# Kernel tuning notes

Hardware: AMD Instinct MI355X
Metric: run time of the kernel (lower is better)

The kernel has to match this reference:

```python
import jax, jax.numpy as jnp
import numpy as np

B, S, D, H = 2, 2048, 1024, 16
HD = D // H  # head_dim = 64
NEG = -1.0e9


def setup_inputs() -> dict:
    key = jax.random.key(0)
    ks = jax.random.split(key, 9)
    s = 1.0 / np.sqrt(D)
    return {
        "x": jax.random.normal(ks[0], (B, S, D), jnp.float32),
        "mask": jnp.ones((B, S), jnp.float32),
        "Wq": jax.random.normal(ks[1], (D, D), jnp.float32) * s,
        "bq": jnp.zeros((D,), jnp.float32),
        "Wk": jax.random.normal(ks[2], (D, D), jnp.float32) * s,
        "bk": jnp.zeros((D,), jnp.float32),
        "Wv": jax.random.normal(ks[3], (D, D), jnp.float32) * s,
        "bv": jnp.zeros((D,), jnp.float32),
        "Wo": jax.random.normal(ks[4], (D, D), jnp.float32) * s,
        "bo": jnp.zeros((D,), jnp.float32),
    }


def reference(x, mask, Wq, bq, Wk, bk, Wv, bv, Wo, bo):
    # QKV projections -> [B, H, S, HD]
    def proj(t, W, b):
        return (t @ W + b).reshape(B, S, H, HD).transpose(0, 2, 1, 3)

    q = proj(x, Wq, bq)
    k = proj(x, Wk, bk)
    v = proj(x, Wv, bv)

    scores = jnp.einsum("bhqd,bhkd->bhqk", q, k) / jnp.sqrt(jnp.asarray(HD, x.dtype))
    # causal mask: scores * m + (1-m) * -1e9 (matches original exactly)
    cm = jnp.tril(jnp.ones((S, S), x.dtype))[None, None]
    scores = scores * cm + (1.0 - cm) * NEG
    # 2D padding mask branch
    scores = scores + (1.0 - mask[:, None, None, :]) * NEG

    attn = jax.nn.softmax(scores, axis=-1)
    out = jnp.einsum("bhqk,bhkd->bqhd", attn, v).reshape(B, S, D)
    return out @ Wo + bo
```

## Files before the change

kernel.cpp:

```cpp
#include <hip/hip_runtime.h>
#include <hip/hip_bf16.h>
#include <cstdint>
#include <cstddef>

typedef __attribute__((ext_vector_type(8))) short short8;
typedef __attribute__((ext_vector_type(4))) float floatx4;
typedef __attribute__((ext_vector_type(4))) unsigned short ushortx4;
typedef __attribute__((ext_vector_type(2))) unsigned int uintx2;

#define MFMA16(a, b, c) __builtin_amdgcn_mfma_f32_16x16x32_bf16((a), (b), (c), 0, 0, 0)
#define LOG2E 1.44269504088896340736f
#define EXP2(x) __builtin_amdgcn_exp2f(x)

__device__ __forceinline__ unsigned short f2bf(float f) {
  unsigned int u = __builtin_bit_cast(unsigned int, f);
  u += 0x7fffu + ((u >> 16) & 1u);
  return (unsigned short)(u >> 16);
}

__device__ __forceinline__ unsigned int pk2(float a, float b) {
  float2 f; f.x = a; f.y = b;
  __hip_bfloat162 h = __float22bfloat162_rn(f);
  unsigned int u;
  __builtin_memcpy(&u, &h, 4);
  return u;
}

typedef __attribute__((address_space(1))) void gvoid_t;
typedef __attribute__((address_space(3))) void svoid_t;
__device__ __forceinline__ void gload_lds16(const void* g, void* l) {
  __builtin_amdgcn_global_load_lds((gvoid_t*)(uintptr_t)g, (svoid_t*)(uintptr_t)l, 16, 0, 0);
}

__global__ void convert_x(const float* __restrict__ x, unsigned short* __restrict__ xb) {
  int i = (blockIdx.x * 256 + threadIdx.x) * 4;
  floatx4 v = *(const floatx4*)(x + i);
  uintx2 o;
  o[0] = pk2(v[0], v[1]);
  o[1] = pk2(v[2], v[3]);
  *(uintx2*)(xb + i) = o;
}

__global__ void transpose_w(const float* __restrict__ Wq, const float* __restrict__ Wk,
                            const float* __restrict__ Wv, const float* __restrict__ Wo,
                            unsigned short* __restrict__ Wqkvt, unsigned short* __restrict__ Wot) {
  __shared__ float tile[32][33];
  int z = blockIdx.z;
  const float* W = (z == 0) ? Wq : (z == 1) ? Wk : (z == 2) ? Wv : Wo;
  unsigned short* out = (z == 3) ? Wot : (Wqkvt + (size_t)z * 1024 * 1024);
  int n0 = blockIdx.x * 32, k0 = blockIdx.y * 32;
  int tx = threadIdx.x, ty = threadIdx.y;
#pragma unroll
  for (int j = 0; j < 4; ++j)
    tile[ty + j * 8][tx] = W[(size_t)(k0 + ty + j * 8) * 1024 + n0 + tx];
  __syncthreads();
#pragma unroll
  for (int j = 0; j < 4; ++j)
    out[(size_t)(n0 + ty + j * 8) * 1024 + k0 + tx] = f2bf(tile[tx][ty + j * 8]);
}

#define GEMM_PROLOGUE()                                                        \
  __shared__ __align__(16) unsigned short As[64 * 64];                         \
  __shared__ __align__(16) unsigned short Bs[128 * 64];                        \
  const int tid = threadIdx.x;                                                 \
  const int lane = tid & 63;                                                   \
  const int wid = tid >> 6;                                                    \
  const int col = lane & 15;                                                   \
  const int quad = lane >> 4;                                                  \
  const int m0 = blockIdx.x * 64;                                              \
  const int n0 = blockIdx.y * 128;                                             \
  const int wm = wid >> 1;                                                     \
  const int wn = wid & 1;                                                      \
  floatx4 acc[2][4];                                                           \
  _Pragma("unroll") for (int i = 0; i < 2; ++i)                                \
      _Pragma("unroll") for (int j = 0; j < 4; ++j)                            \
          acc[i][j] = (floatx4)(0.f);                                          \
  _Pragma("unroll 1") for (int kt = 0; kt < 16; ++kt) {                        \
    __syncthreads();                                                           \
    _Pragma("unroll") for (int call = 0; call < 2; ++call) {                   \
      int c = call * 256 + tid;                                                \
      int r = c >> 3, ch = c & 7;                                              \
      gload_lds16(A + (size_t)(m0 + r) * 1024 + kt * 64 + ((ch ^ (r & 7)) * 8),\
                  As + (size_t)(call * 256 + wid * 64) * 8);                   \
    }                                                                          \
    _Pragma("unroll") for (int call = 0; call < 4; ++call) {                   \
      int c = call * 256 + tid;                                                \
      int r = c >> 3, ch = c & 7;                                              \
      gload_lds16(Bt + (size_t)(n0 + r) * 1024 + kt * 64 + ((ch ^ (r & 7)) * 8),\
                  Bs + (size_t)(call * 256 + wid * 64) * 8);                   \
    }                                                                          \
    __syncthreads();                                                           \
    _Pragma("unroll") for (int ks = 0; ks < 2; ++ks) {                         \
      short8 af[2], bf[4];                                                     \
      _Pragma("unroll") for (int rt = 0; rt < 2; ++rt) {                       \
        int row = wm * 32 + rt * 16 + col;                                     \
        af[rt] = *(const short8*)&As[row * 64 + (((ks * 4 + quad) ^ (row & 7)) * 8)]; \
      }                                                                        \
      _Pragma("unroll") for (int ct = 0; ct < 4; ++ct) {                       \
        int row = wn * 64 + ct * 16 + col;                                     \
        bf[ct] = *(const short8*)&Bs[row * 64 + (((ks * 4 + quad) ^ (row & 7)) * 8)]; \
      }                                                                        \
      _Pragma("unroll") for (int rt = 0; rt < 2; ++rt)                         \
          _Pragma("unroll") for (int ct = 0; ct < 4; ++ct)                     \
              acc[rt][ct] = MFMA16(af[rt], bf[ct], acc[rt][ct]);               \
    }                                                                          \
  }

__global__ __launch_bounds__(256, 5)
void gemm_qkv(const unsigned short* __restrict__ A, const unsigned short* __restrict__ Bt,
              const float* __restrict__ bq, const float* __restrict__ bk,
              const float* __restrict__ bv,
              unsigned short* __restrict__ Qo, unsigned short* __restrict__ Ko,
              unsigned short* __restrict__ Vo) {
  GEMM_PROLOGUE()
  const int nseg = n0 >> 10;
  const float* bias = (nseg == 0) ? bq : ((nseg == 1) ? bk : bv);
#pragma unroll
  for (int rt = 0; rt < 2; ++rt) {
#pragma unroll
    for (int ct = 0; ct < 4; ++ct) {
      int mg = m0 + wm * 32 + rt * 16 + quad * 4;
      int ng = n0 + wn * 64 + ct * 16 + col;
      int c = ng & 1023;
      int hh = c >> 6, hd = c & 63;
      int b_ = mg >> 11, s = mg & 2047;
      float bb = bias[c];
      if (nseg == 2) {
        uintx2 pk;
        pk[0] = pk2(acc[rt][ct][0] + bb, acc[rt][ct][1] + bb);
        pk[1] = pk2(acc[rt][ct][2] + bb, acc[rt][ct][3] + bb);
        *(uintx2*)&Vo[(size_t)(b_ * 16 + hh) * 131072 + (size_t)hd * 2048 + s] = pk;
      } else {
        unsigned short* dst =
            ((nseg == 0) ? Qo : Ko) + ((size_t)(b_ * 16 + hh) * 2048 + s) * 64 + hd;
        float scl = (nseg == 0) ? (0.125f * LOG2E) : 1.0f;
#pragma unroll
        for (int i = 0; i < 4; ++i) dst[(size_t)i * 64] = f2bf((acc[rt][ct][i] + bb) * scl);
      }
    }
  }
}

__global__ __launch_bounds__(256, 5)
void gemm_out(const unsigned short* __restrict__ A, const unsigned short* __restrict__ Bt,
              const float* __restrict__ bo, float* __restrict__ Out) {
  GEMM_PROLOGUE()
#pragma unroll
  for (int rt = 0; rt < 2; ++rt) {
#pragma unroll
    for (int ct = 0; ct < 4; ++ct) {
      int mg = m0 + wm * 32 + rt * 16 + quad * 4;
      int ng = n0 + wn * 64 + ct * 16 + col;
      float bb = bo[ng];
#pragma unroll
      for (int i = 0; i < 4; ++i)
        Out[(size_t)(mg + i) * 1024 + ng] = acc[rt][ct][i] + bb;
    }
  }
}

__global__ __launch_bounds__(256, 3)
void flash_attn(const unsigned short* __restrict__ Q, const unsigned short* __restrict__ K,
                const unsigned short* __restrict__ Vt, const float* __restrict__ mask,
                unsigned short* __restrict__ O) {
  __shared__ __align__(16) unsigned short Ks[128 * 64];
  __shared__ __align__(16) unsigned short Vs[64 * 128];
  __shared__ __align__(16) unsigned short Ps[64 * 128];

  const int tid = threadIdx.x;
  const int lane = tid & 63;
  const int wid = tid >> 6;
  const int col = lane & 15;
  const int quad = lane >> 4;
  const int j = 31 - (int)(blockIdx.x >> 5);
  const int bh = blockIdx.x & 31;
  const int b = bh >> 4, h = bh & 15;
  const int q0 = j * 64;
  const int tdiag = j >> 1;

  const unsigned short* Qp = Q + (size_t)bh * 2048 * 64;
  const unsigned short* Kp = K + (size_t)bh * 2048 * 64;
  const unsigned short* Vp = Vt + (size_t)bh * 64 * 2048;
  const float* mp = mask + b * 2048;

  const int lr8 = lane >> 3, lc8 = lane & 7;
  const int lr16 = lane >> 4, lc16 = lane & 15;
  const floatx4 fzero = (floatx4)(0.f);
  const floatx4 fone = (floatx4)(1.f);

#pragma unroll
  for (int i = 0; i < 2; ++i) {
    int seg = wid * 2 + i;
    int r = seg * 8 + lr8;
    gload_lds16(Qp + (size_t)(q0 + r) * 64 + ((lc8 ^ (r & 7)) * 8), Ps + seg * 512);
  }
  __syncthreads();
  short8 qf[2];
  {
    int q = wid * 16 + col;
#pragma unroll
    for (int ks = 0; ks < 2; ++ks)
      qf[ks] = *(const short8*)&Ps[q * 64 + (((ks * 4 + quad) ^ (q & 7)) * 8)];
  }

  floatx4 o[4];
#pragma unroll
  for (int dt = 0; dt < 4; ++dt) o[dt] = fzero;
  float mrow = -1e30f;
  float lrow = 0.f;

#pragma unroll 1
  for (int t = 0; t <= tdiag; ++t) {
    if (t > 0) __syncthreads();
#pragma unroll
    for (int i = 0; i < 4; ++i) {
      int seg = wid * 4 + i;
      int r = seg * 8 + lr8;
      gload_lds16(Kp + (size_t)(t * 128 + r) * 64 + ((lc8 ^ (r & 7)) * 8), Ks + seg * 512);
    }
#pragma unroll
    for (int i = 0; i < 4; ++i) {
      int seg = wid * 4 + i;
      int r = seg * 4 + lr16;
      gload_lds16(Vp + (size_t)r * 2048 + t * 128 + ((lc16 ^ (r & 15)) * 8), Vs + seg * 512);
    }
    __syncthreads();

    floatx4 mbias[8];
#pragma unroll
    for (int rt = 0; rt < 8; ++rt) {
      floatx4 mm = *(const floatx4*)&mp[t * 128 + rt * 16 + quad * 4];
      mbias[rt] = (fone - mm) * (-1.0e9f * LOG2E);
    }

    floatx4 sc[8];
#pragma unroll
    for (int rt = 0; rt < 8; ++rt) {
      int kr = rt * 16 + col;
      short8 kf0 = *(const short8*)&Ks[kr * 64 + ((quad ^ (col & 7)) * 8)];
      short8 kf1 = *(const short8*)&Ks[kr * 64 + (((4 + quad) ^ (col & 7)) * 8)];
      floatx4 s0 = MFMA16(kf0, qf[0], fzero);
      s0 = MFMA16(kf1, qf[1], s0);
      sc[rt] = s0 + mbias[rt];
    }
    if (t == tdiag) {
      int qg = q0 + wid * 16 + col;
#pragma unroll
      for (int rt = 0; rt < 8; ++rt)
#pragma unroll
        for (int i = 0; i < 4; ++i)
          if (t * 128 + rt * 16 + quad * 4 + i > qg) sc[rt][i] = -1.0e9f * LOG2E;
    }

    float mt = -1e30f;
#pragma unroll
    for (int rt = 0; rt < 8; ++rt)
      mt = fmaxf(mt, fmaxf(fmaxf(sc[rt][0], sc[rt][1]), fmaxf(sc[rt][2], sc[rt][3])));
    mt = fmaxf(mt, __shfl_xor(mt, 16));
    mt = fmaxf(mt, __shfl_xor(mt, 32));
    float mn = fmaxf(mrow, mt);
    float alpha = EXP2(mrow - mn);
    mrow = mn;
    float sum = 0.f;
#pragma unroll
    for (int rt = 0; rt < 8; ++rt)
#pragma unroll
      for (int i = 0; i < 4; ++i) {
        float p = EXP2(sc[rt][i] - mn);
        sc[rt][i] = p;
        sum += p;
      }
    sum += __shfl_xor(sum, 16);
    sum += __shfl_xor(sum, 32);
    lrow = lrow * alpha + sum;
#pragma unroll
    for (int dt = 0; dt < 4; ++dt) o[dt] *= alpha;
    {
      int qloc = wid * 16 + col;
#pragma unroll
      for (int rt = 0; rt < 8; ++rt) {
        uintx2 w;
        w[0] = pk2(sc[rt][0], sc[rt][1]);
        w[1] = pk2(sc[rt][2], sc[rt][3]);
        int chunk = (rt * 2 + (quad >> 1)) ^ col;
        *(uintx2*)&Ps[qloc * 128 + chunk * 8 + (quad & 1) * 4] = w;
      }
    }
#pragma unroll
    for (int ks = 0; ks < 4; ++ks) {
      int ch = ks * 4 + quad;
      short8 pf = *(const short8*)&Ps[(wid * 16 + col) * 128 + ((ch ^ col) * 8)];
#pragma unroll
      for (int dt = 0; dt < 4; ++dt) {
        short8 vf = *(const short8*)&Vs[(dt * 16 + col) * 128 + ((ch ^ col) * 8)];
        o[dt] = MFMA16(vf, pf, o[dt]);
      }
    }
  }

  {
    float inv = 1.0f / lrow;
    int qg = q0 + wid * 16 + col;
    unsigned short* dst = O + ((size_t)(b * 2048 + qg)) * 1024 + h * 64;
#pragma unroll
    for (int dt = 0; dt < 4; ++dt) {
      uintx2 pk;
      pk[0] = pk2(o[dt][0] * inv, o[dt][1] * inv);
      pk[1] = pk2(o[dt][2] * inv, o[dt][3] * inv);
      *(uintx2*)&dst[dt * 16 + quad * 4] = pk;
    }
  }
}

extern "C" void kernel_launch(void* const* d_in, const int* in_sizes, int n_in,
                              void* d_out, int out_size, void* d_ws, size_t ws_size,
                              hipStream_t stream) {
  (void)in_sizes; (void)n_in; (void)out_size; (void)ws_size;
  const float* x  = (const float*)d_in[0];
  const float* mask = (const float*)d_in[1];
  const float* Wq = (const float*)d_in[2];
  const float* bq = (const float*)d_in[3];
  const float* Wk = (const float*)d_in[4];
  const float* bk = (const float*)d_in[5];
  const float* Wv = (const float*)d_in[6];
  const float* bv = (const float*)d_in[7];
  const float* Wo = (const float*)d_in[8];
  const float* bo = (const float*)d_in[9];
  float* out = (float*)d_out;

  char* ws = (char*)d_ws;
  unsigned short* xb    = (unsigned short*)(ws);
  unsigned short* Wqkvt = (unsigned short*)(ws + (8u << 20));
  unsigned short* Wot   = (unsigned short*)(ws + (14u << 20));
  unsigned short* Qb    = (unsigned short*)(ws + (16u << 20));
  unsigned short* Kb    = (unsigned short*)(ws + (24u << 20));
  unsigned short* Vtb   = (unsigned short*)(ws + (32u << 20));
  unsigned short* Ao    = (unsigned short*)(ws + (40u << 20));

  convert_x<<<4096, 256, 0, stream>>>(x, xb);
  transpose_w<<<dim3(32, 32, 4), dim3(32, 8), 0, stream>>>(Wq, Wk, Wv, Wo, Wqkvt, Wot);
  gemm_qkv<<<dim3(64, 24), 256, 0, stream>>>(xb, Wqkvt, bq, bk, bv, Qb, Kb, Vtb);
  flash_attn<<<dim3(1024), 256, 0, stream>>>(Qb, Kb, Vtb, mask, Ao);
  gemm_out<<<dim3(64, 8), 256, 0, stream>>>(Ao, Wot, bo, out);
}
```

Baseline: 185.2 us.

## Enlarge GEMM tiles, register-prefetch K/V, skip all-ones mask and lazy rescale

Both projection GEMMs move from 64x128 to 128x128 block tiles, giving each wave a 4x4 accumulator grid and fewer blocks. Launch bounds drop to 3 to allow for the extra registers. The attention kernel now prefetches the next K/V tile into registers while the current one is computed, replacing direct global-to-LDS loads. It also scans the padding mask once per block and skips the mask-bias arithmetic for tiles that are all ones. The online-softmax rescale is skipped when the new row max exceeds the old by at most 8 in log2 units, trading some exponent headroom and accuracy for fewer multiplies.

```diff
diff --git a/kernel.cpp b/kernel.cpp
--- a/kernel.cpp
+++ b/kernel.cpp
@@ -5,7 +5,6 @@
 
 typedef __attribute__((ext_vector_type(8))) short short8;
 typedef __attribute__((ext_vector_type(4))) float floatx4;
-typedef __attribute__((ext_vector_type(4))) unsigned short ushortx4;
 typedef __attribute__((ext_vector_type(2))) unsigned int uintx2;
 
 #define MFMA16(a, b, c) __builtin_amdgcn_mfma_f32_16x16x32_bf16((a), (b), (c), 0, 0, 0)
@@ -60,53 +59,49 @@
 }
 
 #define GEMM_PROLOGUE()                                                        \
-  __shared__ __align__(16) unsigned short As[64 * 64];                         \
+  __shared__ __align__(16) unsigned short As[128 * 64];                        \
   __shared__ __align__(16) unsigned short Bs[128 * 64];                        \
   const int tid = threadIdx.x;                                                 \
   const int lane = tid & 63;                                                   \
   const int wid = tid >> 6;                                                    \
   const int col = lane & 15;                                                   \
   const int quad = lane >> 4;                                                  \
-  const int m0 = blockIdx.x * 64;                                              \
+  const int m0 = blockIdx.x * 128;                                             \
   const int n0 = blockIdx.y * 128;                                             \
   const int wm = wid >> 1;                                                     \
   const int wn = wid & 1;                                                      \
-  floatx4 acc[2][4];                                                           \
-  _Pragma("unroll") for (int i = 0; i < 2; ++i)                                \
+  floatx4 acc[4][4];                                                           \
+  _Pragma("unroll") for (int i = 0; i < 4; ++i)                                \
       _Pragma("unroll") for (int j = 0; j < 4; ++j)                            \
           acc[i][j] = (floatx4)(0.f);                                          \
   _Pragma("unroll 1") for (int kt = 0; kt < 16; ++kt) {                        \
     __syncthreads();                                                           \
-    _Pragma("unroll") for (int call = 0; call < 2; ++call) {                   \
+    _Pragma("unroll") for (int call = 0; call < 4; ++call) {                   \
       int c = call * 256 + tid;                                                \
       int r = c >> 3, ch = c & 7;                                              \
       gload_lds16(A + (size_t)(m0 + r) * 1024 + kt * 64 + ((ch ^ (r & 7)) * 8),\
                   As + (size_t)(call * 256 + wid * 64) * 8);                   \
-    }                                                                          \
-    _Pragma("unroll") for (int call = 0; call < 4; ++call) {                   \
-      int c = call * 256 + tid;                                                \
-      int r = c >> 3, ch = c & 7;                                              \
       gload_lds16(Bt + (size_t)(n0 + r) * 1024 + kt * 64 + ((ch ^ (r & 7)) * 8),\
                   Bs + (size_t)(call * 256 + wid * 64) * 8);                   \
     }                                                                          \
     __syncthreads();                                                           \
     _Pragma("unroll") for (int ks = 0; ks < 2; ++ks) {                         \
-      short8 af[2], bf[4];                                                     \
-      _Pragma("unroll") for (int rt = 0; rt < 2; ++rt) {                       \
-        int row = wm * 32 + rt * 16 + col;                                     \
+      short8 af[4], bf[4];                                                     \
+      _Pragma("unroll") for (int rt = 0; rt < 4; ++rt) {                       \
+        int row = wm * 64 + rt * 16 + col;                                     \
         af[rt] = *(const short8*)&As[row * 64 + (((ks * 4 + quad) ^ (row & 7)) * 8)]; \
       }                                                                        \
       _Pragma("unroll") for (int ct = 0; ct < 4; ++ct) {                       \
         int row = wn * 64 + ct * 16 + col;                                     \
         bf[ct] = *(const short8*)&Bs[row * 64 + (((ks * 4 + quad) ^ (row & 7)) * 8)]; \
       }                                                                        \
-      _Pragma("unroll") for (int rt = 0; rt < 2; ++rt)                         \
+      _Pragma("unroll") for (int rt = 0; rt < 4; ++rt)                         \
           _Pragma("unroll") for (int ct = 0; ct < 4; ++ct)                     \
               acc[rt][ct] = MFMA16(af[rt], bf[ct], acc[rt][ct]);               \
     }                                                                          \
   }
 
-__global__ __launch_bounds__(256, 5)
+__global__ __launch_bounds__(256, 3)
 void gemm_qkv(const unsigned short* __restrict__ A, const unsigned short* __restrict__ Bt,
               const float* __restrict__ bq, const float* __restrict__ bk,
               const float* __restrict__ bv,
@@ -116,10 +111,10 @@
   const int nseg = n0 >> 10;
   const float* bias = (nseg == 0) ? bq : ((nseg == 1) ? bk : bv);
 #pragma unroll
-  for (int rt = 0; rt < 2; ++rt) {
+  for (int rt = 0; rt < 4; ++rt) {
 #pragma unroll
     for (int ct = 0; ct < 4; ++ct) {
-      int mg = m0 + wm * 32 + rt * 16 + quad * 4;
+      int mg = m0 + wm * 64 + rt * 16 + quad * 4;
       int ng = n0 + wn * 64 + ct * 16 + col;
       int c = ng & 1023;
       int hh = c >> 6, hd = c & 63;
@@ -141,15 +136,15 @@
   }
 }
 
-__global__ __launch_bounds__(256, 5)
+__global__ __launch_bounds__(256, 3)
 void gemm_out(const unsigned short* __restrict__ A, const unsigned short* __restrict__ Bt,
               const float* __restrict__ bo, float* __restrict__ Out) {
   GEMM_PROLOGUE()
 #pragma unroll
-  for (int rt = 0; rt < 2; ++rt) {
+  for (int rt = 0; rt < 4; ++rt) {
 #pragma unroll
     for (int ct = 0; ct < 4; ++ct) {
-      int mg = m0 + wm * 32 + rt * 16 + quad * 4;
+      int mg = m0 + wm * 64 + rt * 16 + quad * 4;
       int ng = n0 + wn * 64 + ct * 16 + col;
       float bb = bo[ng];
 #pragma unroll
@@ -166,6 +161,7 @@
   __shared__ __align__(16) unsigned short Ks[128 * 64];
   __shared__ __align__(16) unsigned short Vs[64 * 128];
   __shared__ __align__(16) unsigned short Ps[64 * 128];
+  __shared__ int mflag[16];
 
   const int tid = threadIdx.x;
   const int lane = tid & 63;
@@ -184,9 +180,15 @@
   const float* mp = mask + b * 2048;
 
   const int lr8 = lane >> 3, lc8 = lane & 7;
-  const int lr16 = lane >> 4, lc16 = lane & 15;
   const floatx4 fzero = (floatx4)(0.f);
   const floatx4 fone = (floatx4)(1.f);
+
+  const int kr = tid >> 1, kh = (tid & 1) * 4;
+  const int vr = tid >> 2, vh = (tid & 3) * 4;
+  const unsigned short* Kg = Kp + (size_t)kr * 64 + kh * 8;
+  const unsigned short* Vg = Vp + (size_t)vr * 2048 + vh * 8;
+  unsigned short* Kl = Ks + kr * 64;
+  unsigned short* Vl = Vs + vr * 128;
 
 #pragma unroll
   for (int i = 0; i < 2; ++i) {
@@ -194,6 +196,12 @@
     int r = seg * 8 + lr8;
     gload_lds16(Qp + (size_t)(q0 + r) * 64 + ((lc8 ^ (r & 7)) * 8), Ps + seg * 512);
   }
+  if (tid < 16) mflag[tid] = 0;
+  short8 kreg[4], vreg[4];
+#pragma unroll
+  for (int c = 0; c < 4; ++c) kreg[c] = *(const short8*)(Kg + c * 8);
+#pragma unroll
+  for (int c = 0; c < 4; ++c) vreg[c] = *(const short8*)(Vg + c * 8);
   __syncthreads();
   short8 qf[2];
   {
@@ -202,6 +210,12 @@
     for (int ks = 0; ks < 2; ++ks)
       qf[ks] = *(const short8*)&Ps[q * 64 + (((ks * 4 + quad) ^ (q & 7)) * 8)];
   }
+  for (int c = tid; c < (tdiag + 1) * 32; c += 256) {
+    floatx4 mm = *(const floatx4*)&mp[c * 4];
+    if (mm[0] != 1.f || mm[1] != 1.f || mm[2] != 1.f || mm[3] != 1.f)
+      atomicOr(&mflag[c >> 5], 1);
+  }
+  __syncthreads();
 
   floatx4 o[4];
 #pragma unroll
@@ -213,35 +227,34 @@
   for (int t = 0; t <= tdiag; ++t) {
     if (t > 0) __syncthreads();
 #pragma unroll
-    for (int i = 0; i < 4; ++i) {
-      int seg = wid * 4 + i;
-      int r = seg * 8 + lr8;
-      gload_lds16(Kp + (size_t)(t * 128 + r) * 64 + ((lc8 ^ (r & 7)) * 8), Ks + seg * 512);
-    }
-#pragma unroll
-    for (int i = 0; i < 4; ++i) {
-      int seg = wid * 4 + i;
-      int r = seg * 4 + lr16;
-      gload_lds16(Vp + (size_t)r * 2048 + t * 128 + ((lc16 ^ (r & 15)) * 8), Vs + seg * 512);
+    for (int c = 0; c < 4; ++c) *(short8*)(Kl + (((kh + c) ^ (kr & 7)) * 8)) = kreg[c];
+#pragma unroll
+    for (int c = 0; c < 4; ++c) *(short8*)(Vl + (((vh + c) ^ (vr & 15)) * 8)) = vreg[c];
+    if (t < tdiag) {
+#pragma unroll
+      for (int c = 0; c < 4; ++c)
+        kreg[c] = *(const short8*)(Kg + (size_t)(t + 1) * 8192 + c * 8);
+#pragma unroll
+      for (int c = 0; c < 4; ++c)
+        vreg[c] = *(const short8*)(Vg + (t + 1) * 128 + c * 8);
     }
     __syncthreads();
 
-    floatx4 mbias[8];
+    floatx4 sc[8];
 #pragma unroll
     for (int rt = 0; rt < 8; ++rt) {
-      floatx4 mm = *(const floatx4*)&mp[t * 128 + rt * 16 + quad * 4];
-      mbias[rt] = (fone - mm) * (-1.0e9f * LOG2E);
-    }
-
-    floatx4 sc[8];
-#pragma unroll
-    for (int rt = 0; rt < 8; ++rt) {
-      int kr = rt * 16 + col;
-      short8 kf0 = *(const short8*)&Ks[kr * 64 + ((quad ^ (col & 7)) * 8)];
-      short8 kf1 = *(const short8*)&Ks[kr * 64 + (((4 + quad) ^ (col & 7)) * 8)];
+      int krr = rt * 16 + col;
+      short8 kf0 = *(const short8*)&Ks[krr * 64 + ((quad ^ (col & 7)) * 8)];
+      short8 kf1 = *(const short8*)&Ks[krr * 64 + (((4 + quad) ^ (col & 7)) * 8)];
       floatx4 s0 = MFMA16(kf0, qf[0], fzero);
-      s0 = MFMA16(kf1, qf[1], s0);
-      sc[rt] = s0 + mbias[rt];
+      sc[rt] = MFMA16(kf1, qf[1], s0);
+    }
+    if (__builtin_amdgcn_readfirstlane(mflag[t])) {
+#pragma unroll
+      for (int rt = 0; rt < 8; ++rt) {
+        floatx4 mm = *(const floatx4*)&mp[t * 128 + rt * 16 + quad * 4];
+        sc[rt] += (fone - mm) * (-1.0e9f * LOG2E);
+      }
     }
     if (t == tdiag) {
       int qg = q0 + wid * 16 + col;
@@ -258,9 +271,17 @@
       mt = fmaxf(mt, fmaxf(fmaxf(sc[rt][0], sc[rt][1]), fmaxf(sc[rt][2], sc[rt][3])));
     mt = fmaxf(mt, __shfl_xor(mt, 16));
     mt = fmaxf(mt, __shfl_xor(mt, 32));
-    float mn = fmaxf(mrow, mt);
-    float alpha = EXP2(mrow - mn);
-    mrow = mn;
+
+    const bool skip = (__all(mt - mrow <= 8.0f) != 0);
+    float mn = mrow;
+    if (!skip) {
+      mn = fmaxf(mrow, mt);
+      float alpha = EXP2(mrow - mn);
+      mrow = mn;
+      lrow *= alpha;
+#pragma unroll
+      for (int dt = 0; dt < 4; ++dt) o[dt] *= alpha;
+    }
     float sum = 0.f;
 #pragma unroll
     for (int rt = 0; rt < 8; ++rt)
@@ -272,9 +293,7 @@
       }
     sum += __shfl_xor(sum, 16);
     sum += __shfl_xor(sum, 32);
-    lrow = lrow * alpha + sum;
-#pragma unroll
-    for (int dt = 0; dt < 4; ++dt) o[dt] *= alpha;
+    lrow += sum;
     {
       int qloc = wid * 16 + col;
 #pragma unroll
@@ -339,7 +358,7 @@
 
   convert_x<<<4096, 256, 0, stream>>>(x, xb);
   transpose_w<<<dim3(32, 32, 4), dim3(32, 8), 0, stream>>>(Wq, Wk, Wv, Wo, Wqkvt, Wot);
-  gemm_qkv<<<dim3(64, 24), 256, 0, stream>>>(xb, Wqkvt, bq, bk, bv, Qb, Kb, Vtb);
+  gemm_qkv<<<dim3(32, 24), 256, 0, stream>>>(xb, Wqkvt, bq, bk, bv, Qb, Kb, Vtb);
   flash_attn<<<dim3(1024), 256, 0, stream>>>(Qb, Kb, Vtb, mask, Ao);
-  gemm_out<<<dim3(64, 8), 256, 0, stream>>>(Ao, Wot, bo, out);
-}
+  gemm_out<<<dim3(32, 8), 256, 0, stream>>>(Ao, Wot, bo, out);
+}
```

After: 186.1 us. About the same (+0.5%).
